# Kernel optimization log

Hardware: AMD Instinct MI355X
Metric: run time of the kernel (lower is better)

Reference implementation:

```python
import jax, jax.numpy as jnp
import numpy as np
import math

B, SQ, SK, H, NH = 8, 512, 512, 768, 12
DH = H // NH

def setup_inputs() -> dict:
    key = jax.random.key(0)
    ks = jax.random.split(key, 8)
    s = 1.0 / math.sqrt(H)
    return {
        "hidden_states": jax.random.normal(ks[0], (B, SQ, H), jnp.float32),
        "context": jax.random.normal(ks[1], (B, SK, H), jnp.float32),
        "attention_mask": jax.random.randint(ks[2], (B, SK), 0, 2, jnp.int32),
        "Wq": jax.random.normal(ks[3], (H, H), jnp.float32) * s,
        "bq": jnp.zeros((H,), jnp.float32),
        "Wk": jax.random.normal(ks[4], (H, H), jnp.float32) * s,
        "bk": jnp.zeros((H,), jnp.float32),
        "Wv": jax.random.normal(ks[5], (H, H), jnp.float32) * s,
        "bv": jnp.zeros((H,), jnp.float32),
        "abs_pos_emb": jax.random.normal(ks[6], (512, DH), jnp.float32),
    }

def _heads(x):
    # [B, S, H] -> [B, NH, S, DH]
    b, s, _ = x.shape
    return x.reshape(b, s, NH, DH).transpose(0, 2, 1, 3)

def reference(hidden_states, context, attention_mask, Wq, bq, Wk, bk, Wv, bv, abs_pos_emb):
    q = _heads(hidden_states @ Wq.T + bq)   # [B,NH,SQ,DH]
    k = _heads(context @ Wk.T + bk)         # [B,NH,SK,DH]
    v = _heads(context @ Wv.T + bv)         # [B,NH,SK,DH]
    scores = jnp.einsum('bhqd,bhkd->bhqk', q, k)
    pos_k = abs_pos_emb[:context.shape[1]]          # [SK, DH]
    pos_q = abs_pos_emb[:hidden_states.shape[1]]    # [SQ, DH]
    pos_scores = jnp.einsum('bhqd,kd->bhqk', q + pos_q[None, None], pos_k)
    scores = (scores + pos_scores) / jnp.sqrt(jnp.float32(DH))
    mask_bias = jnp.where(attention_mask[:, None, None, :] == 0,
                          -jnp.inf, 0.0).astype(scores.dtype)
    scores = scores + mask_bias
    probs = jax.nn.softmax(scores, axis=-1)  # dropout is identity in eval
    out = jnp.einsum('bhqk,bhkd->bhqd', probs, v)
    b, _, sq, _ = out.shape
    return out.transpose(0, 2, 1, 3).reshape(b, sq, NH * DH)
```

## Files before the change

### kernel.cpp

```cpp
#include <hip/hip_runtime.h>
#include <hip/hip_bf16.h>
#include <stdint.h>

#define B_   8
#define SQ_  512
#define SK_  512
#define H_   768
#define NH_  12
#define DH_  64
#define BH_  (B_*NH_)
#define M_   (B_*SQ_)
#define NTOT (3*H_)

typedef __attribute__((ext_vector_type(8))) short short8;
typedef __attribute__((ext_vector_type(4))) float floatx4;
typedef __attribute__((ext_vector_type(4))) unsigned int uint4v;
typedef __attribute__((ext_vector_type(4))) unsigned short ushort4v;

#define MFMA16(a, b, c) __builtin_amdgcn_mfma_f32_16x16x32_bf16((a), (b), (c), 0, 0, 0)

__device__ __forceinline__ unsigned short f2b(float f) {
  union { __hip_bfloat16 h; unsigned short u; } c;
  c.h = __float2bfloat16(f);
  return c.u;
}
__device__ __forceinline__ float b2f(unsigned short u) {
  union { float f; unsigned u; } c; c.u = ((unsigned)u) << 16;
  return c.f;
}
__device__ __forceinline__ short8 ld8(const unsigned short* p) {
  union { uint4v u; short8 s; } c;
  c.u = *(const uint4v*)p;
  return c.s;
}
__device__ __forceinline__ unsigned cvt2(float a, float b) {
  union { __hip_bfloat162 h; unsigned u; } c;
  c.h = __float22bfloat162_rn(float2{a, b});
  return c.u;
}
__device__ __forceinline__ ushort4v cvt4(floatx4 v) {
  union { unsigned u[2]; ushort4v s; } c;
  c.u[0] = cvt2(v.x, v.y);
  c.u[1] = cvt2(v.z, v.w);
  return c.s;
}
__device__ __forceinline__ void gl_lds16(const unsigned short* g, unsigned short* l) {
  __builtin_amdgcn_global_load_lds(
      (const __attribute__((address_space(1))) unsigned int*)g,
      (__attribute__((address_space(3))) unsigned int*)l, 16, 0, 0);
}

#define SEG_X   (M_*H_)
#define SEG_XC  (2*SEG_X)
#define SEG_W1  (H_*H_)
#define SEG_WE  (SEG_XC + 3*SEG_W1)
#define SEG_BE  (SEG_WE + NTOT)
#define SEG_PE  (SEG_BE + SQ_*DH_)

__global__ __launch_bounds__(256) void pack_kernel(
    const float* __restrict__ hid, const float* __restrict__ ctx,
    const float* __restrict__ Wq, const float* __restrict__ Wk, const float* __restrict__ Wv,
    const float* __restrict__ bq, const float* __restrict__ bk, const float* __restrict__ bv,
    const float* __restrict__ pos,
    unsigned short* __restrict__ Xh, unsigned short* __restrict__ Xc,
    unsigned short* __restrict__ Wa, float* __restrict__ Ba,
    unsigned short* __restrict__ Pb)
{
  int i = (blockIdx.x * 256 + threadIdx.x) * 4;
  if (i < SEG_X) {
    floatx4 v = *(const floatx4*)(hid + i);
    *(ushort4v*)(Xh + i) = cvt4(v);
  } else if (i < SEG_XC) {
    int j = i - SEG_X;
    floatx4 v = *(const floatx4*)(ctx + j);
    *(ushort4v*)(Xc + j) = cvt4(v);
  } else if (i < SEG_WE) {
    int j = i - SEG_XC;
    const float* src; int o;
    if (j < SEG_W1)        { src = Wq; o = j; }
    else if (j < 2*SEG_W1) { src = Wk; o = j - SEG_W1; }
    else                   { src = Wv; o = j - 2*SEG_W1; }
    floatx4 v = *(const floatx4*)(src + o);
    *(ushort4v*)(Wa + j) = cvt4(v);
  } else if (i < SEG_BE) {
    int j = i - SEG_WE;
    #pragma unroll
    for (int t = 0; t < 4; ++t) {
      int jj = j + t;
      float v = (jj < H_) ? bq[jj] : (jj < 2*H_) ? bk[jj - H_] : bv[jj - 2*H_];
      Ba[jj] = v;
    }
  } else if (i < SEG_PE) {
    int j = i - SEG_BE;
    floatx4 v = *(const floatx4*)(pos + j);
    *(ushort4v*)(Pb + j) = cvt4(v);
  }
}

__global__ __launch_bounds__(256) void qkv_gemm(
    const unsigned short* __restrict__ Xh, const unsigned short* __restrict__ Xc,
    const unsigned short* __restrict__ W,  const float* __restrict__ bias,
    const unsigned short* __restrict__ Pb,
    unsigned short* __restrict__ qw, unsigned short* __restrict__ kw,
    unsigned short* __restrict__ vt)
{
  __shared__ unsigned short As[2][128][64];
  __shared__ unsigned short Bs[2][128][64];

  int bx = blockIdx.x;
  int xcd = bx & 7, j = bx >> 3;
  int bm = (xcd >> 1) * 8 + j / 9;
  int bn = (xcd & 1) * 9 + j % 9;
  const unsigned short* X = (bn < 6) ? Xh : Xc;
  bool isV = (bn >= 12);
  int m0 = bm * 128, n0 = bn * 128;

  int tid = threadIdx.x;
  int lane = tid & 63, wave = tid >> 6;
  int wm = (wave & 1) * 64, wn = (wave >> 1) * 64;
  int lc16 = lane & 15, quad = lane >> 4, kk = quad * 8;

  int srow = lane >> 3;
  int swz  = (lane & 7) ^ srow;
  int rb   = wave * 32;

  int oa = isV ? wm : wn;
  int ob = isV ? wn : wm;

  floatx4 acc[4][4];
  #pragma unroll
  for (int i = 0; i < 4; ++i)
    #pragma unroll
    for (int jj = 0; jj < 4; ++jj) acc[i][jj] = (floatx4){0.f, 0.f, 0.f, 0.f};

  #pragma unroll
  for (int c = 0; c < 4; ++c) {
    int r = rb + c * 8;
    gl_lds16(&X[(m0 + r + srow) * H_ + swz * 8], &As[0][r][0]);
    gl_lds16(&W[(n0 + r + srow) * H_ + swz * 8], &Bs[0][r][0]);
  }
  __syncthreads();

  for (int t = 0; t < 12; ++t) {
    int cur = t & 1;
    if (t < 11) {
      int k0n = (t + 1) * 64;
      #pragma unroll
      for (int c = 0; c < 4; ++c) {
        int r = rb + c * 8;
        gl_lds16(&X[(m0 + r + srow) * H_ + k0n + swz * 8], &As[cur ^ 1][r][0]);
        gl_lds16(&W[(n0 + r + srow) * H_ + k0n + swz * 8], &Bs[cur ^ 1][r][0]);
      }
    }

    unsigned short (*Acur)[64] = As[cur];
    unsigned short (*Bcur)[64] = Bs[cur];
    unsigned short (*TA)[64] = isV ? Acur : Bcur;
    unsigned short (*TB)[64] = isV ? Bcur : Acur;

    #pragma unroll
    for (int s = 0; s < 2; ++s) {
      short8 af[4], bf[4];
      int key = lc16 & 7;
      int cswz = ((s * 4 + quad) ^ key) * 8;
      #pragma unroll
      for (int i = 0; i < 4; ++i) af[i] = ld8(&TA[oa + i * 16 + lc16][cswz]);
      #pragma unroll
      for (int i = 0; i < 4; ++i) bf[i] = ld8(&TB[ob + i * 16 + lc16][cswz]);
      #pragma unroll
      for (int mi = 0; mi < 4; ++mi)
        #pragma unroll
        for (int ni = 0; ni < 4; ++ni)
          acc[mi][ni] = MFMA16(af[mi], bf[ni], acc[mi][ni]);
    }
    __syncthreads();
  }

  if (!isV) {
    #pragma unroll
    for (int mi = 0; mi < 4; ++mi) {
      #pragma unroll
      for (int ni = 0; ni < 4; ++ni) {
        int gn0 = n0 + wn + mi * 16 + quad * 4;
        int gs  = m0 + wm + ni * 16 + lc16;
        int bidx = gs >> 9, s0 = gs & 511;
        floatx4 bv4 = *(const floatx4*)&bias[gn0];
        if (gn0 < H_) {
          int h = gn0 >> 6, d0 = gn0 & 63;
          floatx4 v;
          #pragma unroll
          for (int r = 0; r < 4; ++r) v[r] = acc[mi][ni][r] + bv4[r];
          *(ushort4v*)(qw + (((bidx * NH_ + h) << 9) + s0) * DH_ + d0) = cvt4(v);
        } else {
          int g = gn0 - H_;
          int h = g >> 6, d0 = g & 63;
          ushort4v pk = *(const ushort4v*)(Pb + s0 * DH_ + d0);
          floatx4 v;
          #pragma unroll
          for (int r = 0; r < 4; ++r) v[r] = acc[mi][ni][r] + bv4[r] + b2f(pk[r]);
          *(ushort4v*)(kw + (((bidx * NH_ + h) << 9) + s0) * DH_ + d0) = cvt4(v);
        }
      }
    }
  } else {
    #pragma unroll
    for (int mi = 0; mi < 4; ++mi) {
      #pragma unroll
      for (int ni = 0; ni < 4; ++ni) {
        int gm0 = m0 + wm + mi * 16 + quad * 4;
        int gn  = n0 + wn + ni * 16 + lc16;
        float bvs = bias[gn];
        int bidx = gm0 >> 9, s0 = gm0 & 511;
        int g = gn - 2 * H_;
        int h = g >> 6, d = g & 63;
        floatx4 v;
        #pragma unroll
        for (int r = 0; r < 4; ++r) v[r] = acc[mi][ni][r] + bvs;
        *(ushort4v*)(vt + ((bidx * NH_ + h) * DH_ + d) * SK_ + s0) = cvt4(v);
      }
    }
  }
}

#define SCALE2 0.18033688011112042f
#define CPAD 136

__global__ __launch_bounds__(256) void attn_kernel(
    const unsigned short* __restrict__ qw, const unsigned short* __restrict__ kw,
    const unsigned short* __restrict__ vt, const unsigned short* __restrict__ posb,
    const int* __restrict__ mask, float* __restrict__ out)
{
  __shared__ unsigned short Sc[2][64][CPAD];
  __shared__ float mb2[SK_];
  __shared__ float red[64][4];

  int bx = blockIdx.x;
  int bh = bx % 96, qt = bx / 96;
  int b = bh / NH_, h = bh - b * NH_;
  int tid = threadIdx.x, lane = tid & 63, wave = tid >> 6;
  int lc16 = lane & 15, quad = lane >> 4, kk = quad * 8;

  for (int i = tid; i < SK_; i += 256)
    mb2[i] = mask[(b << 9) + i] ? 0.0f : -100000.0f;

  const unsigned short* qbase = qw + ((bh << 9) + qt * 64) * DH_;
  const unsigned short* pqb   = posb + (qt * 64) * DH_;
  short8 aq[4][2], ap[4][2];
  #pragma unroll
  for (int rt = 0; rt < 4; ++rt) {
    const unsigned short* qr = qbase + (rt * 16 + lc16) * DH_;
    const unsigned short* pr = pqb + (rt * 16 + lc16) * DH_;
    aq[rt][0] = ld8(qr + kk);
    aq[rt][1] = ld8(qr + 32 + kk);
    ap[rt][0] = ld8(pr + kk);
    ap[rt][1] = ld8(pr + 32 + kk);
  }

  const unsigned short* kwb = kw + ((bh << 9)) * DH_;
  const unsigned short* vb0 = vt + (bh * DH_ + wave * 16 + lc16) * SK_;
  float rs[4] = {0.f, 0.f, 0.f, 0.f};
  floatx4 o[4];
  #pragma unroll
  for (int i = 0; i < 4; ++i) o[i] = (floatx4){0.f, 0.f, 0.f, 0.f};

  short8 cb0, cb1, cp0, cp1, nb0, nb1, np0, np1;
  {
    int kcol = wave * 32;
    const unsigned short* kb = kwb + kcol * DH_;
    const unsigned short* pb = posb + kcol * DH_;
    cb0 = ld8(kb + lc16 * DH_ + kk);
    cb1 = ld8(kb + lc16 * DH_ + 32 + kk);
    cp0 = ld8(pb + lc16 * DH_ + kk);
    cp1 = ld8(pb + lc16 * DH_ + 32 + kk);
  }

  __syncthreads();

  for (int chunk = 0; chunk < 4; ++chunk) {
    unsigned short (*S)[CPAD] = Sc[chunk & 1];

    short8 vf[4];
    #pragma unroll
    for (int ks = 0; ks < 4; ++ks) vf[ks] = ld8(vb0 + chunk * 128 + ks * 32 + kk);

    #pragma unroll
    for (int ct = 0; ct < 2; ++ct) {
      int s = chunk * 2 + ct;
      if (s < 7) {
        int kcol = ((s + 1) >> 1) * 128 + wave * 32 + ((s + 1) & 1) * 16;
        const unsigned short* kb = kwb + kcol * DH_;
        const unsigned short* pb = posb + kcol * DH_;
        nb0 = ld8(kb + lc16 * DH_ + kk);
        nb1 = ld8(kb + lc16 * DH_ + 32 + kk);
        np0 = ld8(pb + lc16 * DH_ + kk);
        np1 = ld8(pb + lc16 * DH_ + 32 + kk);
      }
      int kcol = chunk * 128 + wave * 32 + ct * 16;
      floatx4 mk = *(const floatx4*)&mb2[kcol + quad * 4];
      floatx4 c[4];
      __builtin_amdgcn_s_setprio(1);
      #pragma unroll
      for (int rt = 0; rt < 4; ++rt) {
        c[rt] = (floatx4){0.f, 0.f, 0.f, 0.f};
        c[rt] = MFMA16(cb0, aq[rt][0], c[rt]);
        c[rt] = MFMA16(cb1, aq[rt][1], c[rt]);
        c[rt] = MFMA16(cp0, ap[rt][0], c[rt]);
        c[rt] = MFMA16(cp1, ap[rt][1], c[rt]);
      }
      __builtin_amdgcn_s_setprio(0);
      int lcol = wave * 32 + ct * 16 + quad * 4;
      #pragma unroll
      for (int rt = 0; rt < 4; ++rt) {
        ushort4v pv;
        float sum = 0.f;
        #pragma unroll
        for (int r = 0; r < 4; ++r) {
          float e = __builtin_exp2f(c[rt][r] * SCALE2 + mk[r]);
          sum += e;
          pv[r] = f2b(e);
        }
        rs[rt] += sum;
        *(ushort4v*)&S[rt * 16 + lc16][lcol] = pv;
      }
      cb0 = nb0; cb1 = nb1; cp0 = np0; cp1 = np1;
    }
    __syncthreads();

    __builtin_amdgcn_s_setprio(1);
    #pragma unroll
    for (int ks = 0; ks < 4; ++ks) {
      #pragma unroll
      for (int rt = 0; rt < 4; ++rt) {
        short8 pa = ld8(&S[rt * 16 + lc16][ks * 32 + kk]);
        o[rt] = MFMA16(pa, vf[ks], o[rt]);
      }
    }
    __builtin_amdgcn_s_setprio(0);
  }

  #pragma unroll
  for (int rt = 0; rt < 4; ++rt) {
    rs[rt] += __shfl_xor(rs[rt], 16, 64);
    rs[rt] += __shfl_xor(rs[rt], 32, 64);
  }
  if (quad == 0) {
    #pragma unroll
    for (int rt = 0; rt < 4; ++rt) red[rt * 16 + lc16][wave] = rs[rt];
  }
  __syncthreads();

  #pragma unroll
  for (int rt = 0; rt < 4; ++rt) {
    #pragma unroll
    for (int r = 0; r < 4; ++r) {
      int sl = rt * 16 + quad * 4 + r;
      float inv = 1.0f / (red[sl][0] + red[sl][1] + red[sl][2] + red[sl][3]);
      int s = qt * 64 + sl;
      out[((b << 9) + s) * H_ + h * DH_ + wave * 16 + lc16] = o[rt][r] * inv;
    }
  }
}

extern "C" void kernel_launch(void* const* d_in, const int* in_sizes, int n_in,
                              void* d_out, int out_size, void* d_ws, size_t ws_size,
                              hipStream_t stream) {
  (void)in_sizes; (void)n_in; (void)out_size; (void)ws_size;
  const float* hid  = (const float*)d_in[0];
  const float* ctx  = (const float*)d_in[1];
  const int*   mask = (const int*)d_in[2];
  const float* Wq   = (const float*)d_in[3];
  const float* bq   = (const float*)d_in[4];
  const float* Wk   = (const float*)d_in[5];
  const float* bk   = (const float*)d_in[6];
  const float* Wv   = (const float*)d_in[7];
  const float* bv   = (const float*)d_in[8];
  const float* pos  = (const float*)d_in[9];

  char* ws = (char*)d_ws;
  size_t off = 0;
  auto alloc = [&](size_t bytes) { char* p = ws + off; off = (off + bytes + 255) & ~(size_t)255; return p; };
  unsigned short* Xh = (unsigned short*)alloc((size_t)SEG_X * 2);
  unsigned short* Xc = (unsigned short*)alloc((size_t)SEG_X * 2);
  unsigned short* Wa = (unsigned short*)alloc((size_t)3 * SEG_W1 * 2);
  float*          Ba = (float*)alloc((size_t)NTOT * 4);
  unsigned short* qw = (unsigned short*)alloc((size_t)BH_ * SQ_ * DH_ * 2);
  unsigned short* kw = (unsigned short*)alloc((size_t)BH_ * SK_ * DH_ * 2);
  unsigned short* vt = (unsigned short*)alloc((size_t)BH_ * DH_ * SK_ * 2);
  unsigned short* Pb = (unsigned short*)alloc((size_t)SQ_ * DH_ * 2);

  int pack_blocks = (SEG_PE / 4 + 255) / 256;
  pack_kernel<<<pack_blocks, 256, 0, stream>>>(hid, ctx, Wq, Wk, Wv, bq, bk, bv, pos, Xh, Xc, Wa, Ba, Pb);
  qkv_gemm<<<32 * 18, 256, 0, stream>>>(Xh, Xc, Wa, Ba, Pb, qw, kw, vt);
  attn_kernel<<<BH_ * 8, 256, 0, stream>>>(qw, kw, vt, Pb, mask, (float*)d_out);
}
```

Baseline: 159.3 us.

## Precompute position-position score matrix once and restage QKV GEMM loads through registers

```diff
diff --git a/kernel.cpp b/kernel.cpp
--- a/kernel.cpp
+++ b/kernel.cpp
@@ -43,11 +43,6 @@
   c.u[0] = cvt2(v.x, v.y);
   c.u[1] = cvt2(v.z, v.w);
   return c.s;
-}
-__device__ __forceinline__ void gl_lds16(const unsigned short* g, unsigned short* l) {
-  __builtin_amdgcn_global_load_lds(
-      (const __attribute__((address_space(1))) unsigned int*)g,
-      (__attribute__((address_space(3))) unsigned int*)l, 16, 0, 0);
 }
 
 #define SEG_X   (M_*H_)
@@ -102,12 +97,43 @@
     const unsigned short* __restrict__ W,  const float* __restrict__ bias,
     const unsigned short* __restrict__ Pb,
     unsigned short* __restrict__ qw, unsigned short* __restrict__ kw,
-    unsigned short* __restrict__ vt)
+    unsigned short* __restrict__ vt, float* __restrict__ P2)
 {
-  __shared__ unsigned short As[2][128][64];
-  __shared__ unsigned short Bs[2][128][64];
+  __shared__ unsigned short As[128][72];
+  __shared__ unsigned short Bs[128][72];
 
   int bx = blockIdx.x;
+  int tid = threadIdx.x;
+  int lane = tid & 63, wave = tid >> 6;
+  int lc16 = lane & 15, quad = lane >> 4, kk = quad * 8;
+
+  if (bx >= 576) {
+    int pb = bx - 576;
+    int q0 = (pb >> 2) * 128, k0 = (pb & 3) * 128;
+    int wq = (wave & 1) * 64, wk = (wave >> 1) * 64;
+    short8 aqf[4][2], akf[4][2];
+    #pragma unroll
+    for (int i = 0; i < 4; ++i) {
+      const unsigned short* qr = Pb + (q0 + wq + i * 16 + lc16) * DH_;
+      const unsigned short* kr = Pb + (k0 + wk + i * 16 + lc16) * DH_;
+      aqf[i][0] = ld8(qr + kk);      aqf[i][1] = ld8(qr + 32 + kk);
+      akf[i][0] = ld8(kr + kk);      akf[i][1] = ld8(kr + 32 + kk);
+    }
+    #pragma unroll
+    for (int i = 0; i < 4; ++i) {
+      #pragma unroll
+      for (int jt = 0; jt < 4; ++jt) {
+        floatx4 acc2 = (floatx4){0.f, 0.f, 0.f, 0.f};
+        acc2 = MFMA16(aqf[i][0], akf[jt][0], acc2);
+        acc2 = MFMA16(aqf[i][1], akf[jt][1], acc2);
+        #pragma unroll
+        for (int r = 0; r < 4; ++r)
+          P2[(size_t)(q0 + wq + i * 16 + quad * 4 + r) * SK_ + (k0 + wk + jt * 16 + lc16)] = acc2[r];
+      }
+    }
+    return;
+  }
+
   int xcd = bx & 7, j = bx >> 3;
   int bm = (xcd >> 1) * 8 + j / 9;
   int bn = (xcd & 1) * 9 + j % 9;
@@ -115,15 +141,11 @@
   bool isV = (bn >= 12);
   int m0 = bm * 128, n0 = bn * 128;
 
-  int tid = threadIdx.x;
-  int lane = tid & 63, wave = tid >> 6;
   int wm = (wave & 1) * 64, wn = (wave >> 1) * 64;
-  int lc16 = lane & 15, quad = lane >> 4, kk = quad * 8;
-
-  int srow = lane >> 3;
-  int swz  = (lane & 7) ^ srow;
-  int rb   = wave * 32;
-
+  int srow = tid >> 3, sch = (tid & 7) * 8;
+
+  unsigned short (*TA)[72] = isV ? As : Bs;
+  unsigned short (*TB)[72] = isV ? Bs : As;
   int oa = isV ? wm : wn;
   int ob = isV ? wn : wm;
 
@@ -133,47 +155,43 @@
     #pragma unroll
     for (int jj = 0; jj < 4; ++jj) acc[i][jj] = (floatx4){0.f, 0.f, 0.f, 0.f};
 
-  #pragma unroll
-  for (int c = 0; c < 4; ++c) {
-    int r = rb + c * 8;
-    gl_lds16(&X[(m0 + r + srow) * H_ + swz * 8], &As[0][r][0]);
-    gl_lds16(&W[(n0 + r + srow) * H_ + swz * 8], &Bs[0][r][0]);
-  }
-  __syncthreads();
-
-  for (int t = 0; t < 12; ++t) {
-    int cur = t & 1;
-    if (t < 11) {
-      int k0n = (t + 1) * 64;
-      #pragma unroll
-      for (int c = 0; c < 4; ++c) {
-        int r = rb + c * 8;
-        gl_lds16(&X[(m0 + r + srow) * H_ + k0n + swz * 8], &As[cur ^ 1][r][0]);
-        gl_lds16(&W[(n0 + r + srow) * H_ + k0n + swz * 8], &Bs[cur ^ 1][r][0]);
-      }
-    }
-
-    unsigned short (*Acur)[64] = As[cur];
-    unsigned short (*Bcur)[64] = Bs[cur];
-    unsigned short (*TA)[64] = isV ? Acur : Bcur;
-    unsigned short (*TB)[64] = isV ? Bcur : Acur;
+  uint4v a[4], b[4];
+  #pragma unroll
+  for (int rp = 0; rp < 4; ++rp) {
+    a[rp] = *(const uint4v*)&X[(m0 + srow + rp * 32) * H_ + sch];
+    b[rp] = *(const uint4v*)&W[(n0 + srow + rp * 32) * H_ + sch];
+  }
+
+  for (int k0 = 0; k0 < H_; k0 += 64) {
+    __syncthreads();
+    #pragma unroll
+    for (int rp = 0; rp < 4; ++rp) {
+      *(uint4v*)&As[srow + rp * 32][sch] = a[rp];
+      *(uint4v*)&Bs[srow + rp * 32][sch] = b[rp];
+    }
+    __syncthreads();
+
+    if (k0 + 64 < H_) {
+      #pragma unroll
+      for (int rp = 0; rp < 4; ++rp) {
+        a[rp] = *(const uint4v*)&X[(m0 + srow + rp * 32) * H_ + k0 + 64 + sch];
+        b[rp] = *(const uint4v*)&W[(n0 + srow + rp * 32) * H_ + k0 + 64 + sch];
+      }
+    }
 
     #pragma unroll
     for (int s = 0; s < 2; ++s) {
       short8 af[4], bf[4];
-      int key = lc16 & 7;
-      int cswz = ((s * 4 + quad) ^ key) * 8;
-      #pragma unroll
-      for (int i = 0; i < 4; ++i) af[i] = ld8(&TA[oa + i * 16 + lc16][cswz]);
-      #pragma unroll
-      for (int i = 0; i < 4; ++i) bf[i] = ld8(&TB[ob + i * 16 + lc16][cswz]);
+      #pragma unroll
+      for (int i = 0; i < 4; ++i) af[i] = ld8(&TA[oa + i * 16 + lc16][s * 32 + kk]);
+      #pragma unroll
+      for (int i = 0; i < 4; ++i) bf[i] = ld8(&TB[ob + i * 16 + lc16][s * 32 + kk]);
       #pragma unroll
       for (int mi = 0; mi < 4; ++mi)
         #pragma unroll
         for (int ni = 0; ni < 4; ++ni)
           acc[mi][ni] = MFMA16(af[mi], bf[ni], acc[mi][ni]);
     }
-    __syncthreads();
   }
 
   if (!isV) {
@@ -227,7 +245,7 @@
 
 __global__ __launch_bounds__(256) void attn_kernel(
     const unsigned short* __restrict__ qw, const unsigned short* __restrict__ kw,
-    const unsigned short* __restrict__ vt, const unsigned short* __restrict__ posb,
+    const unsigned short* __restrict__ vt, const float* __restrict__ P2,
     const int* __restrict__ mask, float* __restrict__ out)
 {
   __shared__ unsigned short Sc[2][64][CPAD];
@@ -244,34 +262,32 @@
     mb2[i] = mask[(b << 9) + i] ? 0.0f : -100000.0f;
 
   const unsigned short* qbase = qw + ((bh << 9) + qt * 64) * DH_;
-  const unsigned short* pqb   = posb + (qt * 64) * DH_;
-  short8 aq[4][2], ap[4][2];
+  short8 aq[4][2];
   #pragma unroll
   for (int rt = 0; rt < 4; ++rt) {
     const unsigned short* qr = qbase + (rt * 16 + lc16) * DH_;
-    const unsigned short* pr = pqb + (rt * 16 + lc16) * DH_;
     aq[rt][0] = ld8(qr + kk);
     aq[rt][1] = ld8(qr + 32 + kk);
-    ap[rt][0] = ld8(pr + kk);
-    ap[rt][1] = ld8(pr + 32 + kk);
   }
 
   const unsigned short* kwb = kw + ((bh << 9)) * DH_;
   const unsigned short* vb0 = vt + (bh * DH_ + wave * 16 + lc16) * SK_;
+  const float* p2b = P2 + (size_t)(qt * 64 + lc16) * SK_ + quad * 4;
   float rs[4] = {0.f, 0.f, 0.f, 0.f};
   floatx4 o[4];
   #pragma unroll
   for (int i = 0; i < 4; ++i) o[i] = (floatx4){0.f, 0.f, 0.f, 0.f};
 
-  short8 cb0, cb1, cp0, cp1, nb0, nb1, np0, np1;
+  short8 cb0, cb1, nb0, nb1;
+  floatx4 pc[4], pn[4];
   {
     int kcol = wave * 32;
     const unsigned short* kb = kwb + kcol * DH_;
-    const unsigned short* pb = posb + kcol * DH_;
     cb0 = ld8(kb + lc16 * DH_ + kk);
     cb1 = ld8(kb + lc16 * DH_ + 32 + kk);
-    cp0 = ld8(pb + lc16 * DH_ + kk);
-    cp1 = ld8(pb + lc16 * DH_ + 32 + kk);
+    #pragma unroll
+    for (int rt = 0; rt < 4; ++rt)
+      pc[rt] = *(const floatx4*)(p2b + rt * 16 * SK_ + kcol);
   }
 
   __syncthreads();
@@ -289,11 +305,11 @@
       if (s < 7) {
         int kcol = ((s + 1) >> 1) * 128 + wave * 32 + ((s + 1) & 1) * 16;
         const unsigned short* kb = kwb + kcol * DH_;
-        const unsigned short* pb = posb + kcol * DH_;
         nb0 = ld8(kb + lc16 * DH_ + kk);
         nb1 = ld8(kb + lc16 * DH_ + 32 + kk);
-        np0 = ld8(pb + lc16 * DH_ + kk);
-        np1 = ld8(pb + lc16 * DH_ + 32 + kk);
+        #pragma unroll
+        for (int rt = 0; rt < 4; ++rt)
+          pn[rt] = *(const floatx4*)(p2b + rt * 16 * SK_ + kcol);
       }
       int kcol = chunk * 128 + wave * 32 + ct * 16;
       floatx4 mk = *(const floatx4*)&mb2[kcol + quad * 4];
@@ -301,28 +317,28 @@
       __builtin_amdgcn_s_setprio(1);
       #pragma unroll
       for (int rt = 0; rt < 4; ++rt) {
-        c[rt] = (floatx4){0.f, 0.f, 0.f, 0.f};
+        c[rt] = pc[rt];
         c[rt] = MFMA16(cb0, aq[rt][0], c[rt]);
         c[rt] = MFMA16(cb1, aq[rt][1], c[rt]);
-        c[rt] = MFMA16(cp0, ap[rt][0], c[rt]);
-        c[rt] = MFMA16(cp1, ap[rt][1], c[rt]);
       }
       __builtin_amdgcn_s_setprio(0);
       int lcol = wave * 32 + ct * 16 + quad * 4;
       #pragma unroll
       for (int rt = 0; rt < 4; ++rt) {
-        ushort4v pv;
+        floatx4 ev;
         float sum = 0.f;
         #pragma unroll
         for (int r = 0; r < 4; ++r) {
           float e = __builtin_exp2f(c[rt][r] * SCALE2 + mk[r]);
           sum += e;
-          pv[r] = f2b(e);
+          ev[r] = e;
         }
         rs[rt] += sum;
-        *(ushort4v*)&S[rt * 16 + lc16][lcol] = pv;
-      }
-      cb0 = nb0; cb1 = nb1; cp0 = np0; cp1 = np1;
+        *(ushort4v*)&S[rt * 16 + lc16][lcol] = cvt4(ev);
+      }
+      cb0 = nb0; cb1 = nb1;
+      #pragma unroll
+      for (int rt = 0; rt < 4; ++rt) pc[rt] = pn[rt];
     }
     __syncthreads();
 
@@ -387,9 +403,10 @@
   unsigned short* kw = (unsigned short*)alloc((size_t)BH_ * SK_ * DH_ * 2);
   unsigned short* vt = (unsigned short*)alloc((size_t)BH_ * DH_ * SK_ * 2);
   unsigned short* Pb = (unsigned short*)alloc((size_t)SQ_ * DH_ * 2);
+  float*          P2 = (float*)alloc((size_t)SQ_ * SK_ * 4);
 
   int pack_blocks = (SEG_PE / 4 + 255) / 256;
   pack_kernel<<<pack_blocks, 256, 0, stream>>>(hid, ctx, Wq, Wk, Wv, bq, bk, bv, pos, Xh, Xc, Wa, Ba, Pb);
-  qkv_gemm<<<32 * 18, 256, 0, stream>>>(Xh, Xc, Wa, Ba, Pb, qw, kw, vt);
-  attn_kernel<<<BH_ * 8, 256, 0, stream>>>(qw, kw, vt, Pb, mask, (float*)d_out);
-}
+  qkv_gemm<<<32 * 18 + 16, 256, 0, stream>>>(Xh, Xc, Wa, Ba, Pb, qw, kw, vt, P2);
+  attn_kernel<<<BH_ * 8, 256, 0, stream>>>(qw, kw, vt, P2, mask, (float*)d_out);
+}
```

Measured after the change: 155.4 us. 2.4% less time.

## Replace direct-to-LDS double buffering with register-staged prefetch and padded LDS in QKV GEMM

Applied to the files above, without the earlier changes.

```diff
diff --git a/kernel.cpp b/kernel.cpp
--- a/kernel.cpp
+++ b/kernel.cpp
@@ -43,11 +43,6 @@
   c.u[0] = cvt2(v.x, v.y);
   c.u[1] = cvt2(v.z, v.w);
   return c.s;
-}
-__device__ __forceinline__ void gl_lds16(const unsigned short* g, unsigned short* l) {
-  __builtin_amdgcn_global_load_lds(
-      (const __attribute__((address_space(1))) unsigned int*)g,
-      (__attribute__((address_space(3))) unsigned int*)l, 16, 0, 0);
 }
 
 #define SEG_X   (M_*H_)
@@ -104,8 +99,8 @@
     unsigned short* __restrict__ qw, unsigned short* __restrict__ kw,
     unsigned short* __restrict__ vt)
 {
-  __shared__ unsigned short As[2][128][64];
-  __shared__ unsigned short Bs[2][128][64];
+  __shared__ unsigned short As[128][72];
+  __shared__ unsigned short Bs[128][72];
 
   int bx = blockIdx.x;
   int xcd = bx & 7, j = bx >> 3;
@@ -119,11 +114,10 @@
   int lane = tid & 63, wave = tid >> 6;
   int wm = (wave & 1) * 64, wn = (wave >> 1) * 64;
   int lc16 = lane & 15, quad = lane >> 4, kk = quad * 8;
-
-  int srow = lane >> 3;
-  int swz  = (lane & 7) ^ srow;
-  int rb   = wave * 32;
-
+  int srow = tid >> 3, sch = (tid & 7) * 8;
+
+  unsigned short (*TA)[72] = isV ? As : Bs;
+  unsigned short (*TB)[72] = isV ? Bs : As;
   int oa = isV ? wm : wn;
   int ob = isV ? wn : wm;
 
@@ -133,47 +127,68 @@
     #pragma unroll
     for (int jj = 0; jj < 4; ++jj) acc[i][jj] = (floatx4){0.f, 0.f, 0.f, 0.f};
 
-  #pragma unroll
-  for (int c = 0; c < 4; ++c) {
-    int r = rb + c * 8;
-    gl_lds16(&X[(m0 + r + srow) * H_ + swz * 8], &As[0][r][0]);
-    gl_lds16(&W[(n0 + r + srow) * H_ + swz * 8], &Bs[0][r][0]);
-  }
-  __syncthreads();
+  const unsigned short* Xb = X + (size_t)(m0 + srow) * H_ + sch;
+  const unsigned short* Wb = W + (size_t)(n0 + srow) * H_ + sch;
+
+  uint4v a0[4], b0[4], a1[4], b1[4];
+  #pragma unroll
+  for (int rp = 0; rp < 4; ++rp) {
+    a0[rp] = *(const uint4v*)(Xb + rp * 32 * H_);
+    b0[rp] = *(const uint4v*)(Wb + rp * 32 * H_);
+  }
+  #pragma unroll
+  for (int rp = 0; rp < 4; ++rp) {
+    a1[rp] = *(const uint4v*)(Xb + rp * 32 * H_ + 64);
+    b1[rp] = *(const uint4v*)(Wb + rp * 32 * H_ + 64);
+  }
 
   for (int t = 0; t < 12; ++t) {
-    int cur = t & 1;
-    if (t < 11) {
-      int k0n = (t + 1) * 64;
-      #pragma unroll
-      for (int c = 0; c < 4; ++c) {
-        int r = rb + c * 8;
-        gl_lds16(&X[(m0 + r + srow) * H_ + k0n + swz * 8], &As[cur ^ 1][r][0]);
-        gl_lds16(&W[(n0 + r + srow) * H_ + k0n + swz * 8], &Bs[cur ^ 1][r][0]);
-      }
-    }
-
-    unsigned short (*Acur)[64] = As[cur];
-    unsigned short (*Bcur)[64] = Bs[cur];
-    unsigned short (*TA)[64] = isV ? Acur : Bcur;
-    unsigned short (*TB)[64] = isV ? Bcur : Acur;
+    __syncthreads();
+    if (t & 1) {
+      #pragma unroll
+      for (int rp = 0; rp < 4; ++rp) {
+        *(uint4v*)&As[srow + rp * 32][sch] = a1[rp];
+        *(uint4v*)&Bs[srow + rp * 32][sch] = b1[rp];
+      }
+    } else {
+      #pragma unroll
+      for (int rp = 0; rp < 4; ++rp) {
+        *(uint4v*)&As[srow + rp * 32][sch] = a0[rp];
+        *(uint4v*)&Bs[srow + rp * 32][sch] = b0[rp];
+      }
+    }
+    __syncthreads();
+
+    if (t + 2 < 12) {
+      int kc = (t + 2) * 64;
+      if (t & 1) {
+        #pragma unroll
+        for (int rp = 0; rp < 4; ++rp) {
+          a1[rp] = *(const uint4v*)(Xb + rp * 32 * H_ + kc);
+          b1[rp] = *(const uint4v*)(Wb + rp * 32 * H_ + kc);
+        }
+      } else {
+        #pragma unroll
+        for (int rp = 0; rp < 4; ++rp) {
+          a0[rp] = *(const uint4v*)(Xb + rp * 32 * H_ + kc);
+          b0[rp] = *(const uint4v*)(Wb + rp * 32 * H_ + kc);
+        }
+      }
+    }
 
     #pragma unroll
     for (int s = 0; s < 2; ++s) {
       short8 af[4], bf[4];
-      int key = lc16 & 7;
-      int cswz = ((s * 4 + quad) ^ key) * 8;
-      #pragma unroll
-      for (int i = 0; i < 4; ++i) af[i] = ld8(&TA[oa + i * 16 + lc16][cswz]);
-      #pragma unroll
-      for (int i = 0; i < 4; ++i) bf[i] = ld8(&TB[ob + i * 16 + lc16][cswz]);
+      #pragma unroll
+      for (int i = 0; i < 4; ++i) af[i] = ld8(&TA[oa + i * 16 + lc16][s * 32 + kk]);
+      #pragma unroll
+      for (int i = 0; i < 4; ++i) bf[i] = ld8(&TB[ob + i * 16 + lc16][s * 32 + kk]);
       #pragma unroll
       for (int mi = 0; mi < 4; ++mi)
         #pragma unroll
         for (int ni = 0; ni < 4; ++ni)
           acc[mi][ni] = MFMA16(af[mi], bf[ni], acc[mi][ni]);
     }
-    __syncthreads();
   }
 
   if (!isV) {
@@ -298,7 +313,6 @@
       int kcol = chunk * 128 + wave * 32 + ct * 16;
       floatx4 mk = *(const floatx4*)&mb2[kcol + quad * 4];
       floatx4 c[4];
-      __builtin_amdgcn_s_setprio(1);
       #pragma unroll
       for (int rt = 0; rt < 4; ++rt) {
         c[rt] = (floatx4){0.f, 0.f, 0.f, 0.f};
@@ -307,7 +321,6 @@
         c[rt] = MFMA16(cp0, ap[rt][0], c[rt]);
         c[rt] = MFMA16(cp1, ap[rt][1], c[rt]);
       }
-      __builtin_amdgcn_s_setprio(0);
       int lcol = wave * 32 + ct * 16 + quad * 4;
       #pragma unroll
       for (int rt = 0; rt < 4; ++rt) {
@@ -326,7 +339,6 @@
     }
     __syncthreads();
 
-    __builtin_amdgcn_s_setprio(1);
     #pragma unroll
     for (int ks = 0; ks < 4; ++ks) {
       #pragma unroll
@@ -335,7 +347,6 @@
         o[rt] = MFMA16(pa, vf[ks], o[rt]);
       }
     }
-    __builtin_amdgcn_s_setprio(0);
   }
 
   #pragma unroll
```

New measurement: 166.8 us. +4.7%, slower.
